# Optimization experiments

Hardware: AMD Instinct MI355X
Metric: run time of the kernel (lower is better)

The kernel has to match this reference:

```python
import jax, jax.numpy as jnp
import numpy as np

N_BONDS = 50000
N_EDGES = 600000
BOND_DIM = 64
SPH_DIM = 64
UNITS = 64


def setup_inputs() -> dict:
    key = jax.random.key(0)
    k1, k2, k3, k4, k5 = jax.random.split(key, 5)
    bond_features = jax.random.normal(k1, (N_BONDS, BOND_DIM), dtype=jnp.float32)
    edges_sph_features = jax.random.normal(k2, (N_EDGES, SPH_DIM), dtype=jnp.float32)
    # column 0: sorted segment ids (tf.math.segment_sum requires sorted ids)
    seg = jnp.sort(jax.random.randint(k3, (N_EDGES,), 0, N_BONDS, dtype=jnp.int32))
    nbr = jax.random.randint(k4, (N_EDGES,), 0, N_BONDS, dtype=jnp.int32)
    edges_neighbor = jnp.stack([seg, nbr], axis=1)  # [n_edges, 2]
    kernel = jax.random.normal(k5, (BOND_DIM + SPH_DIM, UNITS), dtype=jnp.float32) * 0.05
    bias = jnp.zeros((UNITS,), dtype=jnp.float32)
    return {
        "bond_features": bond_features,
        "edges_sph_features": edges_sph_features,
        "edges_neighbor": edges_neighbor,
        "kernel": kernel,
        "bias": bias,
    }


def reference(bond_features, edges_sph_features, edges_neighbor, kernel, bias):
    # gather bond features of the neighboring bond for each edge (line-graph)
    gathered = bond_features[edges_neighbor[:, 1]]            # [E, bond_dim]
    concated = jnp.concatenate([gathered, edges_sph_features], axis=-1)  # [E, bond_dim+sph_dim]
    # scatter-reduce into segments (sorted ids; fixed num_segments for jit)
    aggregated = jax.ops.segment_sum(
        concated, edges_neighbor[:, 0], num_segments=N_BONDS,
        indices_are_sorted=True,
    )  # [n_bonds, bond_dim+sph_dim]
    return aggregated @ kernel + bias
```

## Files before the change

kernel.cpp:

```cpp
#include <hip/hip_runtime.h>

#define N_BONDS 50000
#define N_EDGES 600000
#define R_BONDS 4
#define THREADS 512
#define BONDS_PER_BLOCK 32
#define STARTS_BLOCKS ((N_EDGES + 255) / 256)
#define PREMUL_BLOCKS ((N_BONDS + 31) / 32)

typedef float f4 __attribute__((ext_vector_type(4)));
typedef unsigned short u16x4 __attribute__((ext_vector_type(4)));

__device__ __forceinline__ float bcastf(float v, int l) {
    return __builtin_bit_cast(float, __builtin_amdgcn_readlane(__builtin_bit_cast(int, v), l));
}
__device__ __forceinline__ f4 f4zero() { return (f4){0.f, 0.f, 0.f, 0.f}; }
__device__ __forceinline__ void fma4(f4& a, float s, const f4& b) {
    a.x = fmaf(s, b.x, a.x); a.y = fmaf(s, b.y, a.y);
    a.z = fmaf(s, b.z, a.z); a.w = fmaf(s, b.w, a.w);
}
__device__ __forceinline__ float bf2f(unsigned short u) {
    return __builtin_bit_cast(float, ((unsigned)u) << 16);
}
__device__ __forceinline__ unsigned short f2bf(float f) {
    unsigned u = __builtin_bit_cast(unsigned, f);
    return (unsigned short)((u + 0x7fffu + ((u >> 16) & 1u)) >> 16);
}
__device__ __forceinline__ f4 cvt4(u16x4 u) {
    return (f4){bf2f(u.x), bf2f(u.y), bf2f(u.z), bf2f(u.w)};
}

__global__ __launch_bounds__(256)
void prep(const int* __restrict__ edges, int* __restrict__ starts,
          const float* __restrict__ bond, const float* __restrict__ Kmat,
          unsigned short* __restrict__ bondKb) {
    __shared__ float ldsK[64 * 64];
    const int tid = threadIdx.x;

    if (blockIdx.x < STARTS_BLOCKS) {
        const int e = blockIdx.x * 256 + tid;
        if (e >= N_EDGES) return;
        const int2* edges2 = (const int2*)edges;
        const int s  = edges2[e].x;
        const int sp = (e == 0) ? -1 : edges2[e - 1].x;
        for (int b = sp + 1; b <= s; ++b) starts[b] = e;
        if (e == N_EDGES - 1)
            for (int b = s + 1; b <= N_BONDS; ++b) starts[b] = N_EDGES;
        return;
    }

    const int bid  = blockIdx.x - STARTS_BLOCKS;
    const int lane = tid & 63;
    const int wid  = tid >> 6;
    {
        const f4* K4 = (const f4*)Kmat;
        f4* L4 = (f4*)ldsK;
        #pragma unroll
        for (int i = 0; i < 4; ++i) L4[tid + i * 256] = K4[tid + i * 256];
    }
    __syncthreads();
    const int row0 = bid * 32 + wid * 8;
    if (row0 >= N_BONDS) return;

    float rowv[8], acc[8];
    #pragma unroll
    for (int r = 0; r < 8; ++r) {
        int ri = row0 + r; if (ri >= N_BONDS) ri = N_BONDS - 1;
        rowv[r] = bond[ri * 64 + lane];
        acc[r]  = 0.f;
    }
    #pragma unroll 4
    for (int d = 0; d < 64; ++d) {
        const float k = ldsK[d * 64 + lane];
        #pragma unroll
        for (int r = 0; r < 8; ++r)
            acc[r] = fmaf(bcastf(rowv[r], d), k, acc[r]);
    }
    #pragma unroll
    for (int r = 0; r < 8; ++r)
        if (row0 + r < N_BONDS)
            bondKb[(row0 + r) * 64 + lane] = f2bf(acc[r]);
}

__global__ __launch_bounds__(THREADS, 4)
void fused_gather_segsum_mm(const unsigned short* __restrict__ bondKb,
                            const float* __restrict__ sph,
                            const int*   __restrict__ edges,
                            const float* __restrict__ Kmat,
                            const float* __restrict__ bias,
                            const int*   __restrict__ starts,
                            float* __restrict__ out)
{
    __shared__ float ldsK[64 * 64];
    const int tid  = threadIdx.x;
    const int lane = tid & 63;
    const int wid  = tid >> 6;
    const int fl   = lane & 15;
    const int sg   = lane >> 4;

    {
        const f4* K4 = (const f4*)Kmat;
        f4*       L4 = (f4*)ldsK;
        #pragma unroll
        for (int i = 0; i < 2; ++i) L4[tid + i * THREADS] = K4[1024 + tid + i * THREADS];
    }
    __syncthreads();

    const int b0 = blockIdx.x * BONDS_PER_BLOCK + wid * R_BONDS;
    if (b0 >= N_BONDS) return;

    int st[R_BONDS + 1];
    #pragma unroll
    for (int r = 0; r <= R_BONDS; ++r)
        st[r] = __builtin_amdgcn_readfirstlane(starts[b0 + r]);

    const int eb    = st[0];
    const int total = st[R_BONDS] - eb;

    const u16x4* bk4    = (const u16x4*)bondKb;
    const f4*    sph4   = (const f4*)sph;
    const int2*  edges2 = (const int2*)edges;

    float slotG[R_BONDS], slotS[R_BONDS];
    f4 aG = f4zero(), aS = f4zero();
    int r = 0, cs = 0, bnd = st[1] - eb;

    auto txr = [&](f4 v) -> float {
        v.x += __shfl_xor(v.x, 16); v.y += __shfl_xor(v.y, 16);
        v.z += __shfl_xor(v.z, 16); v.w += __shfl_xor(v.w, 16);
        v.x += __shfl_xor(v.x, 32); v.y += __shfl_xor(v.y, 32);
        v.z += __shfl_xor(v.z, 32); v.w += __shfl_xor(v.w, 32);
        const int src = lane >> 2;
        const float s0 = __shfl(v.x, src), s1 = __shfl(v.y, src);
        const float s2 = __shfl(v.z, src), s3 = __shfl(v.w, src);
        const float r01 = (lane & 1) ? s1 : s0;
        const float r23 = (lane & 1) ? s3 : s2;
        return (lane & 2) ? r23 : r01;
    };

    auto slowpath = [&](int q, f4 GV, f4 SV) {
        const int qe = q + sg;
        while (true) {
            const float m = (qe >= cs && qe < bnd) ? 1.f : 0.f;
            fma4(aG, m, GV); fma4(aS, m, SV);
            if (bnd > q + 4) break;
            const float tG = txr(aG), tS = txr(aS);
            #pragma unroll
            for (int rr = 0; rr < R_BONDS; ++rr)
                if (rr == r) { slotG[rr] = tG; slotS[rr] = tS; }
            aG = f4zero(); aS = f4zero();
            cs = bnd;
            ++r;
            if (r >= R_BONDS) { bnd = 0x7fffffff; break; }
            #pragma unroll
            for (int rr = 2; rr <= R_BONDS; ++rr)
                if (r + 1 == rr) bnd = st[rr] - eb;
        }
    };

    int w0 = 0;
    while (w0 < total) {
        int wlen = total - w0; if (wlen > 64) wlen = 64;
        int2 p = make_int2(0, 0);
        if (lane < wlen) p = edges2[eb + w0 + lane];
        const int ng = (wlen + 3) >> 2;

        u16x4 uA, uB, uC, uD;
        f4 sA, sB, sC, sD;

#define ISS(QQ, UV, SV) do { \
        if ((QQ) < ng) { \
            const int idx_ = (QQ) * 4 + sg; \
            const int nbr_ = __shfl(p.y, idx_); \
            int qe_ = w0 + idx_; if (qe_ >= total) qe_ = total - 1; \
            UV = bk4[nbr_ * 16 + fl]; \
            SV = sph4[(eb + qe_) * 16 + fl]; \
        } else { UV = (u16x4){0,0,0,0}; SV = f4zero(); } } while (0)

#define ACC(QQ, UV, SV) do { \
        const int q_ = w0 + (QQ) * 4; \
        const f4 GVf = cvt4(UV); \
        if (q_ + 4 <= bnd) { aG += GVf; aS += SV; } \
        else slowpath(q_, GVf, SV); } while (0)

        ISS(0, uA, sA); ISS(1, uB, sB); ISS(2, uC, sC); ISS(3, uD, sD);
        int q = 0;
        for (; q + 4 <= ng; q += 4) {
            ACC(q + 0, uA, sA); ISS(q + 4, uA, sA);
            ACC(q + 1, uB, sB); ISS(q + 5, uB, sB);
            ACC(q + 2, uC, sC); ISS(q + 6, uC, sC);
            ACC(q + 3, uD, sD); ISS(q + 7, uD, sD);
        }
        if (q + 0 < ng) ACC(q + 0, uA, sA);
        if (q + 1 < ng) ACC(q + 1, uB, sB);
        if (q + 2 < ng) ACC(q + 2, uC, sC);
#undef ISS
#undef ACC
        w0 += wlen;
    }

    {
        const float tG = txr(aG), tS = txr(aS);
        #pragma unroll
        for (int rr = 0; rr < R_BONDS; ++rr) {
            if (rr == r)     { slotG[rr] = tG;  slotS[rr] = tS; }
            else if (rr > r) { slotG[rr] = 0.f; slotS[rr] = 0.f; }
        }
    }

    float acc[R_BONDS];
    const float bl = bias[lane];
    #pragma unroll
    for (int rr = 0; rr < R_BONDS; ++rr) acc[rr] = slotG[rr] + bl;

    #pragma unroll 4
    for (int d = 0; d < 64; ++d) {
        const float kb = ldsK[d * 64 + lane];
        #pragma unroll
        for (int rr = 0; rr < R_BONDS; ++rr)
            acc[rr] = fmaf(bcastf(slotS[rr], d), kb, acc[rr]);
    }

    #pragma unroll
    for (int rr = 0; rr < R_BONDS; ++rr)
        if (b0 + rr < N_BONDS)
            __builtin_nontemporal_store(acc[rr], &out[(b0 + rr) * 64 + lane]);
}

extern "C" void kernel_launch(void* const* d_in, const int* in_sizes, int n_in,
                              void* d_out, int out_size, void* d_ws, size_t ws_size,
                              hipStream_t stream) {
    const float* bond  = (const float*)d_in[0];
    const float* sph   = (const float*)d_in[1];
    const int*   edges = (const int*)d_in[2];
    const float* Kmat  = (const float*)d_in[3];
    const float* bias  = (const float*)d_in[4];
    float* out = (float*)d_out;

    int*            starts = (int*)d_ws;
    unsigned short* bondKb = (unsigned short*)((char*)d_ws + 262144);

    prep<<<STARTS_BLOCKS + PREMUL_BLOCKS, 256, 0, stream>>>(edges, starts,
                                                            bond, Kmat, bondKb);

    const int nblocks = (N_BONDS + BONDS_PER_BLOCK - 1) / BONDS_PER_BLOCK;
    fused_gather_segsum_mm<<<nblocks, THREADS, 0, stream>>>(bondKb, sph, edges, Kmat,
                                                            bias, starts, out);
}
```

Measured before the change: 75.84 us.

## Stage sph rows into double-buffered LDS via async global-to-LDS loads

The main kernel now uses 256-thread blocks with 4 waves of 8 bonds each. Each block walks its whole contiguous edge range in 32-edge windows. The sph rows for each window are loaded into double-buffered shared memory with global_load_lds while the bondK gather is issued from registers, and all waves share the window and sync each iteration. The goal is to overlap the streaming sph loads with gather and accumulate work and to make those loads cooperative. In exchange it adds block-wide barriers per window, makes every wave process every edge in the block range even when it belongs to other waves' bonds, and uses more LDS, which may lower occupancy.

```diff
diff --git a/kernel.cpp b/kernel.cpp
--- a/kernel.cpp
+++ b/kernel.cpp
@@ -1,12 +1,14 @@
 #include <hip/hip_runtime.h>
+#include <stdint.h>
 
 #define N_BONDS 50000
 #define N_EDGES 600000
-#define R_BONDS 4
-#define THREADS 512
+#define GB 8
 #define BONDS_PER_BLOCK 32
+#define WIN 32
 #define STARTS_BLOCKS ((N_EDGES + 255) / 256)
 #define PREMUL_BLOCKS ((N_BONDS + 31) / 32)
+#define MAIN_BLOCKS ((N_BONDS + BONDS_PER_BLOCK - 1) / BONDS_PER_BLOCK)
 
 typedef float f4 __attribute__((ext_vector_type(4)));
 typedef unsigned short u16x4 __attribute__((ext_vector_type(4)));
@@ -82,16 +84,18 @@
             bondKb[(row0 + r) * 64 + lane] = f2bf(acc[r]);
 }
 
-__global__ __launch_bounds__(THREADS, 4)
-void fused_gather_segsum_mm(const unsigned short* __restrict__ bondKb,
-                            const float* __restrict__ sph,
-                            const int*   __restrict__ edges,
-                            const float* __restrict__ Kmat,
-                            const float* __restrict__ bias,
-                            const int*   __restrict__ starts,
-                            float* __restrict__ out)
+__global__ __launch_bounds__(256, 5)
+void fused_staged(const unsigned short* __restrict__ bondKb,
+                  const float* __restrict__ sph,
+                  const int*   __restrict__ edges,
+                  const float* __restrict__ Kmat,
+                  const float* __restrict__ bias,
+                  const int*   __restrict__ starts,
+                  float* __restrict__ out)
 {
     __shared__ float ldsK[64 * 64];
+    __shared__ float sphb[2][WIN * 64];
+
     const int tid  = threadIdx.x;
     const int lane = tid & 63;
     const int wid  = tid >> 6;
@@ -100,30 +104,47 @@
 
     {
         const f4* K4 = (const f4*)Kmat;
-        f4*       L4 = (f4*)ldsK;
-        #pragma unroll
-        for (int i = 0; i < 2; ++i) L4[tid + i * THREADS] = K4[1024 + tid + i * THREADS];
-    }
-    __syncthreads();
-
-    const int b0 = blockIdx.x * BONDS_PER_BLOCK + wid * R_BONDS;
-    if (b0 >= N_BONDS) return;
-
-    int st[R_BONDS + 1];
-    #pragma unroll
-    for (int r = 0; r <= R_BONDS; ++r)
-        st[r] = __builtin_amdgcn_readfirstlane(starts[b0 + r]);
-
-    const int eb    = st[0];
-    const int total = st[R_BONDS] - eb;
-
-    const u16x4* bk4    = (const u16x4*)bondKb;
+        f4* L4 = (f4*)ldsK;
+        #pragma unroll
+        for (int i = 0; i < 4; ++i) L4[tid + i * 256] = K4[1024 + tid + i * 256];
+    }
+
+    const int blkb = blockIdx.x * BONDS_PER_BLOCK;
+    const int b0w  = blkb + wid * GB;
+
+    int st[GB + 1];
+    #pragma unroll
+    for (int r = 0; r <= GB; ++r) {
+        int ix = b0w + r; if (ix > N_BONDS) ix = N_BONDS;
+        st[r] = __builtin_amdgcn_readfirstlane(starts[ix]);
+    }
+    int eblk = blkb + BONDS_PER_BLOCK; if (eblk > N_BONDS) eblk = N_BONDS;
+    const int EB = __builtin_amdgcn_readfirstlane(starts[blkb]);
+    const int EE = __builtin_amdgcn_readfirstlane(starts[eblk]);
+    const int NW = (EE - EB + WIN - 1) / WIN;
+
     const f4*    sph4   = (const f4*)sph;
     const int2*  edges2 = (const int2*)edges;
-
-    float slotG[R_BONDS], slotS[R_BONDS];
+    const u16x4* bk4    = (const u16x4*)bondKb;
+
+    auto stage = [&](int w, int b) {
+        int base = (EB + WIN * w + 8 * wid) * 16;
+        int a0 = base + lane;       if (a0 > N_EDGES * 16 - 1) a0 = N_EDGES * 16 - 1;
+        int a1 = base + 64 + lane;  if (a1 > N_EDGES * 16 - 1) a1 = N_EDGES * 16 - 1;
+        uint32_t* lp0 = (uint32_t*)&sphb[b][wid * 512];
+        uint32_t* lp1 = (uint32_t*)&sphb[b][wid * 512 + 256];
+        __builtin_amdgcn_global_load_lds((const uint32_t*)(sph4 + a0), lp0, 16, 0, 0);
+        __builtin_amdgcn_global_load_lds((const uint32_t*)(sph4 + a1), lp1, 16, 0, 0);
+    };
+    auto loadwin = [&](int w) -> int2 {
+        int e = EB + WIN * w + lane;
+        if (e > N_EDGES - 1) e = N_EDGES - 1;
+        return (lane < WIN) ? edges2[e] : make_int2(0, 0);
+    };
+
+    float slotG[GB], slotS[GB];
     f4 aG = f4zero(), aS = f4zero();
-    int r = 0, cs = 0, bnd = st[1] - eb;
+    int r = 0, csA = st[0], bndA = st[1];
 
     auto txr = [&](f4 v) -> float {
         v.x += __shfl_xor(v.x, 16); v.y += __shfl_xor(v.y, 16);
@@ -138,93 +159,88 @@
         return (lane & 2) ? r23 : r01;
     };
 
-    auto slowpath = [&](int q, f4 GV, f4 SV) {
-        const int qe = q + sg;
+    auto doquad = [&](int E0, f4 gv, f4 sv) {
+        if (E0 + 4 <= csA) return;
+        if (E0 >= csA && E0 + 4 <= bndA) { aG += gv; aS += sv; return; }
+        const int Ee = E0 + sg;
         while (true) {
-            const float m = (qe >= cs && qe < bnd) ? 1.f : 0.f;
-            fma4(aG, m, GV); fma4(aS, m, SV);
-            if (bnd > q + 4) break;
+            const float m = (Ee >= csA && Ee < bndA) ? 1.f : 0.f;
+            fma4(aG, m, gv); fma4(aS, m, sv);
+            if (bndA > E0 + 4) break;
             const float tG = txr(aG), tS = txr(aS);
             #pragma unroll
-            for (int rr = 0; rr < R_BONDS; ++rr)
+            for (int rr = 0; rr < GB; ++rr)
                 if (rr == r) { slotG[rr] = tG; slotS[rr] = tS; }
             aG = f4zero(); aS = f4zero();
-            cs = bnd;
+            csA = bndA;
             ++r;
-            if (r >= R_BONDS) { bnd = 0x7fffffff; break; }
+            if (r >= GB) { bndA = 0x7fffffff; break; }
             #pragma unroll
-            for (int rr = 2; rr <= R_BONDS; ++rr)
-                if (r + 1 == rr) bnd = st[rr] - eb;
+            for (int rr = 2; rr <= GB; ++rr)
+                if (r + 1 == rr) bndA = st[rr];
         }
     };
 
-    int w0 = 0;
-    while (w0 < total) {
-        int wlen = total - w0; if (wlen > 64) wlen = 64;
-        int2 p = make_int2(0, 0);
-        if (lane < wlen) p = edges2[eb + w0 + lane];
-        const int ng = (wlen + 3) >> 2;
-
-        u16x4 uA, uB, uC, uD;
-        f4 sA, sB, sC, sD;
-
-#define ISS(QQ, UV, SV) do { \
-        if ((QQ) < ng) { \
-            const int idx_ = (QQ) * 4 + sg; \
-            const int nbr_ = __shfl(p.y, idx_); \
-            int qe_ = w0 + idx_; if (qe_ >= total) qe_ = total - 1; \
-            UV = bk4[nbr_ * 16 + fl]; \
-            SV = sph4[(eb + qe_) * 16 + fl]; \
-        } else { UV = (u16x4){0,0,0,0}; SV = f4zero(); } } while (0)
-
-#define ACC(QQ, UV, SV) do { \
-        const int q_ = w0 + (QQ) * 4; \
-        const f4 GVf = cvt4(UV); \
-        if (q_ + 4 <= bnd) { aG += GVf; aS += SV; } \
-        else slowpath(q_, GVf, SV); } while (0)
-
-        ISS(0, uA, sA); ISS(1, uB, sB); ISS(2, uC, sC); ISS(3, uD, sD);
-        int q = 0;
-        for (; q + 4 <= ng; q += 4) {
-            ACC(q + 0, uA, sA); ISS(q + 4, uA, sA);
-            ACC(q + 1, uB, sB); ISS(q + 5, uB, sB);
-            ACC(q + 2, uC, sC); ISS(q + 6, uC, sC);
-            ACC(q + 3, uD, sD); ISS(q + 7, uD, sD);
-        }
-        if (q + 0 < ng) ACC(q + 0, uA, sA);
-        if (q + 1 < ng) ACC(q + 1, uB, sB);
-        if (q + 2 < ng) ACC(q + 2, uC, sC);
-#undef ISS
-#undef ACC
-        w0 += wlen;
+    int2 pc = make_int2(0, 0);
+    if (NW > 0) { stage(0, 0); pc = loadwin(0); }
+    __syncthreads();
+
+    int buf = 0;
+    for (int w = 0; w < NW; ++w) {
+        if (w + 1 < NW) stage(w + 1, buf ^ 1);
+        int2 pn = (w + 1 < NW) ? loadwin(w + 1) : make_int2(0, 0);
+
+        const int W0 = EB + WIN * w;
+
+        u16x4 g0 = bk4[__shfl(pc.y,  0 + sg) * 16 + fl];
+        u16x4 g1 = bk4[__shfl(pc.y,  4 + sg) * 16 + fl];
+        u16x4 g2 = bk4[__shfl(pc.y,  8 + sg) * 16 + fl];
+        u16x4 g3 = bk4[__shfl(pc.y, 12 + sg) * 16 + fl];
+        u16x4 g4 = bk4[__shfl(pc.y, 16 + sg) * 16 + fl];
+        u16x4 g5 = bk4[__shfl(pc.y, 20 + sg) * 16 + fl];
+        u16x4 g6 = bk4[__shfl(pc.y, 24 + sg) * 16 + fl];
+        u16x4 g7 = bk4[__shfl(pc.y, 28 + sg) * 16 + fl];
+
+        const f4* sb = (const f4*)&sphb[buf][0];
+        doquad(W0 +  0, cvt4(g0), sb[( 0 + sg) * 16 + fl]);
+        doquad(W0 +  4, cvt4(g1), sb[( 4 + sg) * 16 + fl]);
+        doquad(W0 +  8, cvt4(g2), sb[( 8 + sg) * 16 + fl]);
+        doquad(W0 + 12, cvt4(g3), sb[(12 + sg) * 16 + fl]);
+        doquad(W0 + 16, cvt4(g4), sb[(16 + sg) * 16 + fl]);
+        doquad(W0 + 20, cvt4(g5), sb[(20 + sg) * 16 + fl]);
+        doquad(W0 + 24, cvt4(g6), sb[(24 + sg) * 16 + fl]);
+        doquad(W0 + 28, cvt4(g7), sb[(28 + sg) * 16 + fl]);
+
+        __syncthreads();
+        buf ^= 1; pc = pn;
     }
 
     {
         const float tG = txr(aG), tS = txr(aS);
         #pragma unroll
-        for (int rr = 0; rr < R_BONDS; ++rr) {
+        for (int rr = 0; rr < GB; ++rr) {
             if (rr == r)     { slotG[rr] = tG;  slotS[rr] = tS; }
             else if (rr > r) { slotG[rr] = 0.f; slotS[rr] = 0.f; }
         }
     }
 
-    float acc[R_BONDS];
+    float acc[GB];
     const float bl = bias[lane];
     #pragma unroll
-    for (int rr = 0; rr < R_BONDS; ++rr) acc[rr] = slotG[rr] + bl;
+    for (int rr = 0; rr < GB; ++rr) acc[rr] = slotG[rr] + bl;
 
     #pragma unroll 4
     for (int d = 0; d < 64; ++d) {
         const float kb = ldsK[d * 64 + lane];
         #pragma unroll
-        for (int rr = 0; rr < R_BONDS; ++rr)
+        for (int rr = 0; rr < GB; ++rr)
             acc[rr] = fmaf(bcastf(slotS[rr], d), kb, acc[rr]);
     }
 
     #pragma unroll
-    for (int rr = 0; rr < R_BONDS; ++rr)
-        if (b0 + rr < N_BONDS)
-            __builtin_nontemporal_store(acc[rr], &out[(b0 + rr) * 64 + lane]);
+    for (int rr = 0; rr < GB; ++rr)
+        if (b0w + rr < N_BONDS)
+            __builtin_nontemporal_store(acc[rr], &out[(b0w + rr) * 64 + lane]);
 }
 
 extern "C" void kernel_launch(void* const* d_in, const int* in_sizes, int n_in,
@@ -243,7 +259,6 @@
     prep<<<STARTS_BLOCKS + PREMUL_BLOCKS, 256, 0, stream>>>(edges, starts,
                                                             bond, Kmat, bondKb);
 
-    const int nblocks = (N_BONDS + BONDS_PER_BLOCK - 1) / BONDS_PER_BLOCK;
-    fused_gather_segsum_mm<<<nblocks, THREADS, 0, stream>>>(bondKb, sph, edges, Kmat,
-                                                            bias, starts, out);
-}
+    fused_staged<<<MAIN_BLOCKS, 256, 0, stream>>>(bondKb, sph, edges, Kmat,
+                                                  bias, starts, out);
+}
```

Measured after the change: 127.3 us. +67.8%, slower.
